# Optimization experiments

Measured on AMD Instinct MI355X. Metric: run time of the kernel, lower is better.

The kernel has to match this reference:

```python
import jax, jax.numpy as jnp
import numpy as np

B, S, DM, H = 16, 4096, 512, 4
HD = DM // H  # head_dim = 128
EPS = 1e-5


def setup_inputs() -> dict:
    key = jax.random.key(0)
    ks = jax.random.split(key, 9)
    sc = 1.0 / np.sqrt(DM)
    inp = {
        "x": jax.random.normal(ks[0], (B, S, DM), dtype=jnp.float32),
        "Wq_w": jax.random.normal(ks[1], (DM, DM), dtype=jnp.float32) * sc,
        "Wq_b": jnp.zeros((DM,), dtype=jnp.float32),
        "Wk_w": jax.random.normal(ks[2], (DM, DM), dtype=jnp.float32) * sc,
        "Wk_b": jnp.zeros((DM,), dtype=jnp.float32),
        "Wv_w": jax.random.normal(ks[3], (DM, DM), dtype=jnp.float32) * sc,
        "Wv_b": jnp.zeros((DM,), dtype=jnp.float32),
        "Wo_w": jax.random.normal(ks[4], (DM, DM), dtype=jnp.float32) * sc,
        "Wo_b": jnp.zeros((DM,), dtype=jnp.float32),
        "ln_g": jnp.ones((DM,), dtype=jnp.float32),
        "ln_b": jnp.zeros((DM,), dtype=jnp.float32),
    }
    return inp


def _forward(x, Wq_w, Wq_b, Wk_w, Wk_b, Wv_w, Wv_b, Wo_w, Wo_b, ln_g, ln_b):
    b, s, _ = x.shape
    # Linear projections, viewed as [B,S,H,HD] exactly as the torch code does
    Q = (x @ Wq_w.T + Wq_b).reshape(b, s, H, HD)
    K = (x @ Wk_w.T + Wk_b).reshape(b, s, H, HD)
    V = (x @ Wv_w.T + Wv_b).reshape(b, s, H, HD)
    # NOTE: source never permutes heads to dim 1, so attention is over the
    # HEAD axis per token: scores [B,S,H,H]
    scores = jnp.einsum("bshd,bstd->bsht", Q, K) / np.sqrt(HD).astype(np.float32)
    attn = jax.nn.softmax(scores, axis=-1)  # dropout is identity in eval
    out = jnp.einsum("bsht,bstd->bshd", attn, V).reshape(b, s, DM)
    out = out @ Wo_w.T + Wo_b
    y = out + x  # input_dim == output_dim -> residual branch taken
    mu = jnp.mean(y, axis=-1, keepdims=True)
    var = jnp.mean((y - mu) ** 2, axis=-1, keepdims=True)
    return (y - mu) * jax.lax.rsqrt(var + EPS) * ln_g + ln_b


def reference(x, Wq_w, Wq_b, Wk_w, Wk_b, Wv_w, Wv_b, Wo_w, Wo_b, ln_g, ln_b):
    return _forward(x, Wq_w, Wq_b, Wk_w, Wk_b, Wv_w, Wv_b, Wo_w, Wo_b, ln_g, ln_b)
```

## Files before the change

kernel.cpp:

```cpp
#include <hip/hip_runtime.h>
#include <stdint.h>

#define NTOK 65536
#define DMODEL 512
#define QKVN 1536
#define LN_EPS 1e-5f

typedef __attribute__((ext_vector_type(8))) short short8;
typedef __attribute__((ext_vector_type(8))) unsigned short ushort8;
typedef __attribute__((ext_vector_type(4))) float float4_t;
typedef __attribute__((ext_vector_type(4))) unsigned int uint4_t;

static __device__ __forceinline__ float bf2f(unsigned short u) {
    union { unsigned int i; float f; } c; c.i = ((unsigned int)u) << 16; return c.f;
}
static __device__ __forceinline__ unsigned short f2bf(float f) {
    union { float f; unsigned int i; } c; c.f = f;
    unsigned int x = c.i;
    return (unsigned short)((x + 0x7fffu + ((x >> 16) & 1u)) >> 16);
}
static __device__ __forceinline__ unsigned int cvt_pk_bf16(float lo, float hi) {
    unsigned int r;
    asm("v_cvt_pk_bf16_f32 %0, %1, %2" : "=v"(r) : "v"(lo), "v"(hi));
    return r;
}
static __device__ __forceinline__ void gload_lds16(const void* g, void* l) {
    __builtin_amdgcn_global_load_lds((const __attribute__((address_space(1))) void*)g,
                                     (__attribute__((address_space(3))) void*)l, 16, 0, 0);
}

#define BAR() __builtin_amdgcn_s_barrier()
#define WAITL0() asm volatile("s_waitcnt lgkmcnt(0)" ::: "memory")
#define WVM(n) asm volatile("s_waitcnt vmcnt(" #n ")" ::: "memory")
#define MFMA(a, b, c) __builtin_amdgcn_mfma_f32_16x16x32_bf16((a), (b), (c), 0, 0, 0)

__global__ __launch_bounds__(256) void cast_x_kernel(const float* __restrict__ x,
                                                     unsigned short* __restrict__ xb, int n8) {
    int stride = gridDim.x * blockDim.x;
    for (int i = blockIdx.x * blockDim.x + threadIdx.x; i < n8; i += stride) {
        const float4_t* p = (const float4_t*)(x + (size_t)i * 8);
        float4_t a = p[0], b = p[1];
        ushort8 v;
        v[0] = f2bf(a[0]); v[1] = f2bf(a[1]); v[2] = f2bf(a[2]); v[3] = f2bf(a[3]);
        v[4] = f2bf(b[0]); v[5] = f2bf(b[1]); v[6] = f2bf(b[2]); v[7] = f2bf(b[3]);
        *(ushort8*)(xb + (size_t)i * 8) = v;
    }
}

__global__ __launch_bounds__(256) void prep_w_kernel(
    const float* __restrict__ wq, const float* __restrict__ wk, const float* __restrict__ wv,
    const float* __restrict__ wo,
    const float* __restrict__ bq, const float* __restrict__ bk, const float* __restrict__ bv,
    unsigned short* __restrict__ wqkv, unsigned short* __restrict__ wpack,
    float* __restrict__ bias_qkv) {
    const int WN = DMODEL * DMODEL;
    int tid = blockIdx.x * blockDim.x + threadIdx.x;
    int stride = gridDim.x * blockDim.x;
    for (int j = tid; j < 3 * WN; j += stride) {
        int seg = j / WN, idx = j - seg * WN;
        const float* src = (seg == 0) ? wq : (seg == 1) ? wk : wv;
        wqkv[j] = f2bf(src[idx]);
    }
    for (int j = tid; j < WN; j += stride) {
        int e = j & 7, l = (j >> 3) & 63, nf = (j >> 9) & 31, kt = j >> 14;
        int row = nf * 16 + (l & 15);
        int k = kt * 32 + ((l >> 4) << 3) + e;
        wpack[j] = f2bf(wo[row * 512 + k]);
    }
    for (int j = tid; j < QKVN; j += stride)
        bias_qkv[j] = (j < 512) ? bq[j] : (j < 1024) ? bk[j - 512] : bv[j - 1024];
}

__global__ __launch_bounds__(512, 2) void gemm1_kernel(
    const unsigned short* __restrict__ A, const unsigned short* __restrict__ Bw,
    const float* __restrict__ bias, unsigned short* __restrict__ Cout) {
    __shared__ unsigned short As[4][256 * 32];
    __shared__ unsigned short Bs[4][256 * 32];

    const int b = blockIdx.x;
    const int L = (b & 7) * 192 + (b >> 3);
    const int bm = L / 6;
    const int bn = L - bm * 6;

    const int t = threadIdx.x;
    const int lane = t & 63;
    const int w = t >> 6;
    const int wm = w >> 2, wn = w & 3;

    const unsigned short* Ab = A + (size_t)bm * 256 * 512;
    const unsigned short* Bb = Bw + (size_t)bn * 256 * 512;

    const int i0 = t, i1 = 512 + t;
    const int r0 = i0 >> 2, s0 = (i0 & 3) ^ ((r0 >> 1) & 3);
    const int r1 = i1 >> 2, s1 = (i1 & 3) ^ ((r1 >> 1) & 3);

#define STAGE_A1(kt) do { \
        gload_lds16(Ab + r0 * 512 + (kt) * 32 + s0 * 8, &As[(kt) & 3][i0 * 8]); \
        gload_lds16(Ab + r1 * 512 + (kt) * 32 + s1 * 8, &As[(kt) & 3][i1 * 8]); } while (0)
#define STAGE_B1(kt) do { \
        gload_lds16(Bb + r0 * 512 + (kt) * 32 + s0 * 8, &Bs[(kt) & 3][i0 * 8]); \
        gload_lds16(Bb + r1 * 512 + (kt) * 32 + s1 * 8, &Bs[(kt) & 3][i1 * 8]); } while (0)

    int aoff[8], boff[4];
#pragma unroll
    for (int m = 0; m < 8; m++) {
        int row = wm * 128 + m * 16 + (lane & 15);
        aoff[m] = row * 32 + (((lane >> 4) ^ ((row >> 1) & 3)) * 8);
    }
#pragma unroll
    for (int n = 0; n < 4; n++) {
        int row = wn * 64 + n * 16 + (lane & 15);
        boff[n] = row * 32 + (((lane >> 4) ^ ((row >> 1) & 3)) * 8);
    }

    float4_t acc[8][4];
#pragma unroll
    for (int m = 0; m < 8; m++)
#pragma unroll
        for (int n = 0; n < 4; n++) acc[m][n] = (float4_t){0.f, 0.f, 0.f, 0.f};

    STAGE_A1(0); STAGE_B1(0);
    STAGE_A1(1); STAGE_B1(1);
    STAGE_A1(2); STAGE_B1(2);
    WVM(8);
    BAR();

    short8 ar[8], br[4];
#pragma unroll
    for (int kt = 0; kt < 16; ++kt) {
        const int sl = kt & 3;
#pragma unroll
        for (int m = 0; m < 8; m++) ar[m] = *(const short8*)&As[sl][aoff[m]];
        br[0] = *(const short8*)&Bs[sl][boff[0]];
        br[1] = *(const short8*)&Bs[sl][boff[1]];
        if (kt <= 12) STAGE_A1(kt + 3);
        BAR();
        WAITL0();
        __builtin_amdgcn_s_setprio(1);
#pragma unroll
        for (int m = 0; m < 8; m++) {
            acc[m][0] = MFMA(ar[m], br[0], acc[m][0]);
            acc[m][1] = MFMA(ar[m], br[1], acc[m][1]);
        }
        __builtin_amdgcn_s_setprio(0);
        BAR();
        br[2] = *(const short8*)&Bs[sl][boff[2]];
        br[3] = *(const short8*)&Bs[sl][boff[3]];
        if (kt <= 12) STAGE_B1(kt + 3);
        BAR();
        WAITL0();
        __builtin_amdgcn_s_setprio(1);
#pragma unroll
        for (int m = 0; m < 8; m++) {
            acc[m][2] = MFMA(ar[m], br[2], acc[m][2]);
            acc[m][3] = MFMA(ar[m], br[3], acc[m][3]);
        }
        __builtin_amdgcn_s_setprio(0);
        if (kt <= 12) { WVM(8); }
        else if (kt == 13) { WVM(4); }
        else if (kt == 14) { WVM(0); }
        BAR();
    }

    const int orow0 = bm * 256 + wm * 128;
    const int ocol0 = bn * 256 + wn * 64;
#pragma unroll
    for (int m = 0; m < 8; m++) {
#pragma unroll
        for (int n = 0; n < 4; n++) {
            int col = ocol0 + n * 16 + (lane & 15);
            float bv = bias[col];
#pragma unroll
            for (int j = 0; j < 4; j++) {
                int row = orow0 + m * 16 + (lane >> 4) * 4 + j;
                Cout[(size_t)row * QKVN + col] = f2bf(acc[m][n][j] + bv);
            }
        }
    }
#undef STAGE_A1
#undef STAGE_B1
}

__global__ __launch_bounds__(256, 4) void attn_o_ln_kernel(
    const unsigned short* __restrict__ qkv, const unsigned short* __restrict__ Wpack,
    const float* __restrict__ bo, const float* __restrict__ xres,
    const float* __restrict__ lng, const float* __restrict__ lnb,
    float* __restrict__ Y) {
    __shared__ __align__(16) unsigned char AOs[32 * 1024];
    float* red = (float*)AOs;

    const int T0 = blockIdx.x * 32;
    const int t = threadIdx.x;
    const int lane = t & 63;
    const int w = t >> 6;
    const int g = lane >> 4;
    const int sl = lane & 15;

    const float scale = 0.08838834764831845f;

#pragma unroll 1
    for (int r = 0; r < 2; ++r) {
        const int tr = w * 8 + r * 4 + g;
        const unsigned short* base = qkv + (size_t)(T0 + tr) * QKVN + sl * 8;

        short8 qr[4], kr[4], vr[4];
#pragma unroll
        for (int h = 0; h < 4; h++) {
            qr[h] = *(const short8*)(base + h * 128);
            kr[h] = *(const short8*)(base + 512 + h * 128);
            vr[h] = *(const short8*)(base + 1024 + h * 128);
        }
#pragma unroll
        for (int h = 0; h < 4; h++) {
            float qf[8];
#pragma unroll
            for (int d = 0; d < 8; d++) qf[d] = bf2f((unsigned short)qr[h][d]);
            float s[4];
#pragma unroll
            for (int tt = 0; tt < 4; tt++) {
                float a0 = 0.f;
#pragma unroll
                for (int d = 0; d < 8; d++) a0 += qf[d] * bf2f((unsigned short)kr[tt][d]);
                s[tt] = a0;
            }
#pragma unroll
            for (int mask = 1; mask < 16; mask <<= 1)
#pragma unroll
                for (int tt = 0; tt < 4; tt++)
                    s[tt] += __shfl_xor(s[tt], mask, 64);
            float m0 = fmaxf(fmaxf(s[0], s[1]), fmaxf(s[2], s[3])) * scale;
            float p[4];
            float sum = 0.f;
#pragma unroll
            for (int tt = 0; tt < 4; tt++) { p[tt] = __expf(s[tt] * scale - m0); sum += p[tt]; }
            float rr = __frcp_rn(sum);
            float o[8];
#pragma unroll
            for (int d = 0; d < 8; d++) o[d] = 0.f;
#pragma unroll
            for (int tt = 0; tt < 4; tt++) {
                float ph = p[tt] * rr;
#pragma unroll
                for (int d = 0; d < 8; d++) o[d] += ph * bf2f((unsigned short)vr[tt][d]);
            }
            uint4_t pk;
            pk[0] = cvt_pk_bf16(o[0], o[1]);
            pk[1] = cvt_pk_bf16(o[2], o[3]);
            pk[2] = cvt_pk_bf16(o[4], o[5]);
            pk[3] = cvt_pk_bf16(o[6], o[7]);
            int off = tr * 1024 + ((h * 256 + sl * 16) ^ ((tr & 7) << 4));
            *(uint4_t*)(AOs + off) = pk;
        }
    }
    __syncthreads();

    const unsigned short* Bb2 = Wpack + ((size_t)(w * 8) * 64 + lane) * 8;
    const int arow0 = sl;
    const int arow1 = 16 + sl;

    float4_t acc[2][8];
#pragma unroll
    for (int m = 0; m < 2; m++)
#pragma unroll
        for (int n = 0; n < 8; n++) acc[m][n] = (float4_t){0.f, 0.f, 0.f, 0.f};

#pragma unroll 1
    for (int kt = 0; kt < 16; ++kt) {
        short8 bfr[8];
#pragma unroll
        for (int n = 0; n < 8; n++)
            bfr[n] = *(const short8*)(Bb2 + (size_t)kt * 16384 + n * 512);
        int lslot = kt * 64 + g * 16;
        short8 a0 = *(const short8*)(AOs + arow0 * 1024 + (lslot ^ ((arow0 & 7) << 4)));
        short8 a1 = *(const short8*)(AOs + arow1 * 1024 + (lslot ^ ((arow1 & 7) << 4)));
#pragma unroll
        for (int n = 0; n < 8; n++) {
            acc[0][n] = MFMA(a0, bfr[n], acc[0][n]);
            acc[1][n] = MFMA(a1, bfr[n], acc[1][n]);
        }
    }
    __syncthreads();

    float bias8[8], gc8[8], bc8[8];
#pragma unroll
    for (int n = 0; n < 8; n++) {
        int c = w * 128 + n * 16 + sl;
        bias8[n] = bo[c]; gc8[n] = lng[c]; bc8[n] = lnb[c];
    }
#pragma unroll
    for (int m = 0; m < 2; m++) {
#pragma unroll
        for (int j = 0; j < 4; j++) {
            int grow = T0 + m * 16 + g * 4 + j;
            const float* xr = xres + (size_t)grow * 512;
#pragma unroll
            for (int n = 0; n < 8; n++)
                acc[m][n][j] += bias8[n] + xr[w * 128 + n * 16 + sl];
        }
    }
#pragma unroll
    for (int m = 0; m < 2; m++) {
#pragma unroll
        for (int j = 0; j < 4; j++) {
            float s = 0.f, s2 = 0.f;
#pragma unroll
            for (int n = 0; n < 8; n++) { float v = acc[m][n][j]; s += v; s2 += v * v; }
#pragma unroll
            for (int mask = 1; mask < 16; mask <<= 1) {
                s += __shfl_xor(s, mask, 64);
                s2 += __shfl_xor(s2, mask, 64);
            }
            if (sl == 0) {
                int rl = m * 16 + g * 4 + j;
                red[(rl * 4 + w) * 2 + 0] = s;
                red[(rl * 4 + w) * 2 + 1] = s2;
            }
        }
    }
    __syncthreads();
#pragma unroll
    for (int m = 0; m < 2; m++) {
#pragma unroll
        for (int j = 0; j < 4; j++) {
            int rl = m * 16 + g * 4 + j;
            float s = 0.f, s2 = 0.f;
#pragma unroll
            for (int i = 0; i < 4; i++) {
                s += red[(rl * 4 + i) * 2 + 0];
                s2 += red[(rl * 4 + i) * 2 + 1];
            }
            float mu = s * (1.f / 512.f);
            float var = s2 * (1.f / 512.f) - mu * mu;
            float inv = rsqrtf(var + LN_EPS);
            float* yp = Y + (size_t)(T0 + rl) * 512;
#pragma unroll
            for (int n = 0; n < 8; n++) {
                int c = w * 128 + n * 16 + sl;
                yp[c] = (acc[m][n][j] - mu) * inv * gc8[n] + bc8[n];
            }
        }
    }
}

extern "C" void kernel_launch(void* const* d_in, const int* in_sizes, int n_in,
                              void* d_out, int out_size, void* d_ws, size_t ws_size,
                              hipStream_t stream) {
    const float* x   = (const float*)d_in[0];
    const float* wq  = (const float*)d_in[1];
    const float* bq  = (const float*)d_in[2];
    const float* wk  = (const float*)d_in[3];
    const float* bk  = (const float*)d_in[4];
    const float* wv  = (const float*)d_in[5];
    const float* bv  = (const float*)d_in[6];
    const float* wo  = (const float*)d_in[7];
    const float* bo  = (const float*)d_in[8];
    const float* lng = (const float*)d_in[9];
    const float* lnb = (const float*)d_in[10];

    char* ws = (char*)d_ws;
    unsigned short* Xb    = (unsigned short*)(ws);
    unsigned short* Wqkv  = (unsigned short*)(ws + 67108864);
    unsigned short* Wpack = (unsigned short*)(ws + 68681728);
    float*          Bqkv  = (float*)        (ws + 69206016);
    unsigned short* QKV   = (unsigned short*)(ws + 69212160);
    float* Y = (float*)d_out;

    cast_x_kernel<<<2048, 256, 0, stream>>>(x, Xb, NTOK * 512 / 8);
    prep_w_kernel<<<1024, 256, 0, stream>>>(wq, wk, wv, wo, bq, bk, bv, Wqkv, Wpack, Bqkv);

    gemm1_kernel<<<(NTOK / 256) * (QKVN / 256), 512, 0, stream>>>(Xb, Wqkv, Bqkv, QKV);

    attn_o_ln_kernel<<<NTOK / 32, 256, 0, stream>>>(QKV, Wpack, bo, x, lng, lnb, Y);
}
```

Baseline: 381.3 us.

## Use 512 threads in attn_o_ln kernel, splitting warps over rows and columns

Doubles the block size of the fused attention/out-projection/LayerNorm kernel to 8 waves. Each wave now handles 4 tokens in the head-attention phase and one 16-row by 128-column tile in the MFMA phase, instead of 8 tokens and 32 rows. This halves per-thread accumulators and sequential attention work, lowering register pressure and raising parallelism. The cost is that each wave reloads the Wo fragments for its column slice, doubling B-operand global reads per block. The attention loop also reloads K and V inside the per-head loop, adding redundant loads.

```diff
diff --git a/kernel.cpp b/kernel.cpp
--- a/kernel.cpp
+++ b/kernel.cpp
@@ -181,7 +181,7 @@
 #undef STAGE_B1
 }
 
-__global__ __launch_bounds__(256, 4) void attn_o_ln_kernel(
+__global__ __launch_bounds__(512, 4) void attn_o_ln_kernel(
     const unsigned short* __restrict__ qkv, const unsigned short* __restrict__ Wpack,
     const float* __restrict__ bo, const float* __restrict__ xres,
     const float* __restrict__ lng, const float* __restrict__ lnb,
@@ -195,26 +195,31 @@
     const int w = t >> 6;
     const int g = lane >> 4;
     const int sl = lane & 15;
+    const int wm = w >> 2;
+    const int wn = w & 3;
 
     const float scale = 0.08838834764831845f;
 
-#pragma unroll 1
-    for (int r = 0; r < 2; ++r) {
-        const int tr = w * 8 + r * 4 + g;
+    {
+        const int tr = w * 4 + g;
         const unsigned short* base = qkv + (size_t)(T0 + tr) * QKVN + sl * 8;
 
-        short8 qr[4], kr[4], vr[4];
 #pragma unroll
         for (int h = 0; h < 4; h++) {
-            qr[h] = *(const short8*)(base + h * 128);
-            kr[h] = *(const short8*)(base + 512 + h * 128);
-            vr[h] = *(const short8*)(base + 1024 + h * 128);
-        }
-#pragma unroll
-        for (int h = 0; h < 4; h++) {
+            short8 qr = *(const short8*)(base + h * 128);
+            short8 kr[4];
+            kr[0] = *(const short8*)(base + 512 + h * 128);
+            short8 vr[4];
+            vr[0] = *(const short8*)(base + 1024 + h * 128);
+            kr[1] = kr[0]; vr[1] = vr[0];
+#pragma unroll
+            for (int tt = 0; tt < 4; tt++) {
+                kr[tt] = *(const short8*)(base + 512 + tt * 128);
+                vr[tt] = *(const short8*)(base + 1024 + tt * 128);
+            }
             float qf[8];
 #pragma unroll
-            for (int d = 0; d < 8; d++) qf[d] = bf2f((unsigned short)qr[h][d]);
+            for (int d = 0; d < 8; d++) qf[d] = bf2f((unsigned short)qr[d]);
             float s[4];
 #pragma unroll
             for (int tt = 0; tt < 4; tt++) {
@@ -254,15 +259,12 @@
     }
     __syncthreads();
 
-    const unsigned short* Bb2 = Wpack + ((size_t)(w * 8) * 64 + lane) * 8;
-    const int arow0 = sl;
-    const int arow1 = 16 + sl;
-
-    float4_t acc[2][8];
-#pragma unroll
-    for (int m = 0; m < 2; m++)
-#pragma unroll
-        for (int n = 0; n < 8; n++) acc[m][n] = (float4_t){0.f, 0.f, 0.f, 0.f};
+    const unsigned short* Bb2 = Wpack + ((size_t)(wn * 8) * 64 + lane) * 8;
+    const int arow = wm * 16 + sl;
+
+    float4_t acc[8];
+#pragma unroll
+    for (int n = 0; n < 8; n++) acc[n] = (float4_t){0.f, 0.f, 0.f, 0.f};
 
 #pragma unroll 1
     for (int kt = 0; kt < 16; ++kt) {
@@ -271,73 +273,60 @@
         for (int n = 0; n < 8; n++)
             bfr[n] = *(const short8*)(Bb2 + (size_t)kt * 16384 + n * 512);
         int lslot = kt * 64 + g * 16;
-        short8 a0 = *(const short8*)(AOs + arow0 * 1024 + (lslot ^ ((arow0 & 7) << 4)));
-        short8 a1 = *(const short8*)(AOs + arow1 * 1024 + (lslot ^ ((arow1 & 7) << 4)));
+        short8 a0 = *(const short8*)(AOs + arow * 1024 + (lslot ^ ((arow & 7) << 4)));
+#pragma unroll
+        for (int n = 0; n < 8; n++) acc[n] = MFMA(a0, bfr[n], acc[n]);
+    }
+    __syncthreads();
+
+    float bias8[8], gc8[8], bc8[8];
+#pragma unroll
+    for (int n = 0; n < 8; n++) {
+        int c = wn * 128 + n * 16 + sl;
+        bias8[n] = bo[c]; gc8[n] = lng[c]; bc8[n] = lnb[c];
+    }
+#pragma unroll
+    for (int j = 0; j < 4; j++) {
+        int grow = T0 + wm * 16 + g * 4 + j;
+        const float* xr = xres + (size_t)grow * 512;
+#pragma unroll
+        for (int n = 0; n < 8; n++)
+            acc[n][j] += bias8[n] + xr[wn * 128 + n * 16 + sl];
+    }
+#pragma unroll
+    for (int j = 0; j < 4; j++) {
+        float s = 0.f, s2 = 0.f;
+#pragma unroll
+        for (int n = 0; n < 8; n++) { float v = acc[n][j]; s += v; s2 += v * v; }
+#pragma unroll
+        for (int mask = 1; mask < 16; mask <<= 1) {
+            s += __shfl_xor(s, mask, 64);
+            s2 += __shfl_xor(s2, mask, 64);
+        }
+        if (sl == 0) {
+            int rl = wm * 16 + g * 4 + j;
+            red[(rl * 4 + wn) * 2 + 0] = s;
+            red[(rl * 4 + wn) * 2 + 1] = s2;
+        }
+    }
+    __syncthreads();
+#pragma unroll
+    for (int j = 0; j < 4; j++) {
+        int rl = wm * 16 + g * 4 + j;
+        float s = 0.f, s2 = 0.f;
+#pragma unroll
+        for (int i = 0; i < 4; i++) {
+            s += red[(rl * 4 + i) * 2 + 0];
+            s2 += red[(rl * 4 + i) * 2 + 1];
+        }
+        float mu = s * (1.f / 512.f);
+        float var = s2 * (1.f / 512.f) - mu * mu;
+        float inv = rsqrtf(var + LN_EPS);
+        float* yp = Y + (size_t)(T0 + rl) * 512;
 #pragma unroll
         for (int n = 0; n < 8; n++) {
-            acc[0][n] = MFMA(a0, bfr[n], acc[0][n]);
-            acc[1][n] = MFMA(a1, bfr[n], acc[1][n]);
-        }
-    }
-    __syncthreads();
-
-    float bias8[8], gc8[8], bc8[8];
-#pragma unroll
-    for (int n = 0; n < 8; n++) {
-        int c = w * 128 + n * 16 + sl;
-        bias8[n] = bo[c]; gc8[n] = lng[c]; bc8[n] = lnb[c];
-    }
-#pragma unroll
-    for (int m = 0; m < 2; m++) {
-#pragma unroll
-        for (int j = 0; j < 4; j++) {
-            int grow = T0 + m * 16 + g * 4 + j;
-            const float* xr = xres + (size_t)grow * 512;
-#pragma unroll
-            for (int n = 0; n < 8; n++)
-                acc[m][n][j] += bias8[n] + xr[w * 128 + n * 16 + sl];
-        }
-    }
-#pragma unroll
-    for (int m = 0; m < 2; m++) {
-#pragma unroll
-        for (int j = 0; j < 4; j++) {
-            float s = 0.f, s2 = 0.f;
-#pragma unroll
-            for (int n = 0; n < 8; n++) { float v = acc[m][n][j]; s += v; s2 += v * v; }
-#pragma unroll
-            for (int mask = 1; mask < 16; mask <<= 1) {
-                s += __shfl_xor(s, mask, 64);
-                s2 += __shfl_xor(s2, mask, 64);
-            }
-            if (sl == 0) {
-                int rl = m * 16 + g * 4 + j;
-                red[(rl * 4 + w) * 2 + 0] = s;
-                red[(rl * 4 + w) * 2 + 1] = s2;
-            }
-        }
-    }
-    __syncthreads();
-#pragma unroll
-    for (int m = 0; m < 2; m++) {
-#pragma unroll
-        for (int j = 0; j < 4; j++) {
-            int rl = m * 16 + g * 4 + j;
-            float s = 0.f, s2 = 0.f;
-#pragma unroll
-            for (int i = 0; i < 4; i++) {
-                s += red[(rl * 4 + i) * 2 + 0];
-                s2 += red[(rl * 4 + i) * 2 + 1];
-            }
-            float mu = s * (1.f / 512.f);
-            float var = s2 * (1.f / 512.f) - mu * mu;
-            float inv = rsqrtf(var + LN_EPS);
-            float* yp = Y + (size_t)(T0 + rl) * 512;
-#pragma unroll
-            for (int n = 0; n < 8; n++) {
-                int c = w * 128 + n * 16 + sl;
-                yp[c] = (acc[m][n][j] - mu) * inv * gc8[n] + bc8[n];
-            }
+            int c = wn * 128 + n * 16 + sl;
+            yp[c] = (acc[n][j] - mu) * inv * gc8[n] + bc8[n];
         }
     }
 }
@@ -370,5 +359,5 @@
 
     gemm1_kernel<<<(NTOK / 256) * (QKVN / 256), 512, 0, stream>>>(Xb, Wqkv, Bqkv, QKV);
 
-    attn_o_ln_kernel<<<NTOK / 32, 256, 0, stream>>>(QKV, Wpack, bo, x, lng, lnb, Y);
-}
+    attn_o_ln_kernel<<<NTOK / 32, 512, 0, stream>>>(QKV, Wpack, bo, x, lng, lnb, Y);
+}
```

Result: faster. 333.0 us (-12.7%).

## Stage Wo tiles in double-buffered LDS and widen attention block to 64 tokens

Applied to the files above, without the earlier changes.

The fused attention/output-projection/LayerNorm kernel now handles 64 tokens per block with 8 waves (2x4 wave grid) instead of 32 tokens with 4 waves. Wo is no longer pre-packed for direct per-wave global fragment loads. Instead it is cast to plain bf16 and streamed into swizzled, double-buffered shared memory with async global-to-LDS loads, overlapping the next k-tile load with MFMA work. The aim is to share each Wo tile across two row-groups of waves, halving redundant global/L2 traffic for weights. In exchange it adds per-k-tile barriers and more LDS per block, which can lower occupancy.

```diff
diff --git a/kernel.cpp b/kernel.cpp
--- a/kernel.cpp
+++ b/kernel.cpp
@@ -51,7 +51,7 @@
     const float* __restrict__ wq, const float* __restrict__ wk, const float* __restrict__ wv,
     const float* __restrict__ wo,
     const float* __restrict__ bq, const float* __restrict__ bk, const float* __restrict__ bv,
-    unsigned short* __restrict__ wqkv, unsigned short* __restrict__ wpack,
+    unsigned short* __restrict__ wqkv, unsigned short* __restrict__ wob,
     float* __restrict__ bias_qkv) {
     const int WN = DMODEL * DMODEL;
     int tid = blockIdx.x * blockDim.x + threadIdx.x;
@@ -61,12 +61,7 @@
         const float* src = (seg == 0) ? wq : (seg == 1) ? wk : wv;
         wqkv[j] = f2bf(src[idx]);
     }
-    for (int j = tid; j < WN; j += stride) {
-        int e = j & 7, l = (j >> 3) & 63, nf = (j >> 9) & 31, kt = j >> 14;
-        int row = nf * 16 + (l & 15);
-        int k = kt * 32 + ((l >> 4) << 3) + e;
-        wpack[j] = f2bf(wo[row * 512 + k]);
-    }
+    for (int j = tid; j < WN; j += stride) wob[j] = f2bf(wo[j]);
     for (int j = tid; j < QKVN; j += stride)
         bias_qkv[j] = (j < 512) ? bq[j] : (j < 1024) ? bk[j - 512] : bv[j - 1024];
 }
@@ -181,24 +176,37 @@
 #undef STAGE_B1
 }
 
-__global__ __launch_bounds__(256, 4) void attn_o_ln_kernel(
-    const unsigned short* __restrict__ qkv, const unsigned short* __restrict__ Wpack,
+__global__ __launch_bounds__(512, 2) void attn_gemm_ln_kernel(
+    const unsigned short* __restrict__ qkv, const unsigned short* __restrict__ Wob,
     const float* __restrict__ bo, const float* __restrict__ xres,
     const float* __restrict__ lng, const float* __restrict__ lnb,
     float* __restrict__ Y) {
-    __shared__ __align__(16) unsigned char AOs[32 * 1024];
-    float* red = (float*)AOs;
-
-    const int T0 = blockIdx.x * 32;
+    __shared__ __align__(16) unsigned char AOs[64 * 1024];
+    __shared__ __align__(16) unsigned char Bsm[2][32768];
+    float* red = (float*)Bsm;
+
+    const int T0 = blockIdx.x * 64;
     const int t = threadIdx.x;
     const int lane = t & 63;
     const int w = t >> 6;
     const int g = lane >> 4;
     const int sl = lane & 15;
+    const int wm = w >> 2;
+    const int wn = w & 3;
+
+#define STAGE_B2(kt) do { \
+        _Pragma("unroll") \
+        for (int c = 0; c < 4; c++) { \
+            int idx = c * 512 + t; \
+            int row = idx >> 2; \
+            int s = (idx & 3) ^ ((row >> 1) & 3); \
+            gload_lds16(Wob + row * 512 + (kt) * 32 + s * 8, &Bsm[(kt) & 1][idx * 16]); \
+        } } while (0)
+
+    STAGE_B2(0);
 
     const float scale = 0.08838834764831845f;
-
-#pragma unroll 1
+#pragma unroll
     for (int r = 0; r < 2; ++r) {
         const int tr = w * 8 + r * 4 + g;
         const unsigned short* base = qkv + (size_t)(T0 + tr) * QKVN + sl * 8;
@@ -254,9 +262,16 @@
     }
     __syncthreads();
 
-    const unsigned short* Bb2 = Wpack + ((size_t)(w * 8) * 64 + lane) * 8;
-    const int arow0 = sl;
-    const int arow1 = 16 + sl;
+    const int arow0 = wm * 32 + sl;
+    const int arow1 = wm * 32 + 16 + sl;
+    const int aswz0 = (arow0 & 7) << 4;
+    const int aswz1 = (arow1 & 7) << 4;
+    int boffB[8];
+#pragma unroll
+    for (int n = 0; n < 8; n++) {
+        int row = wn * 128 + n * 16 + sl;
+        boffB[n] = row * 64 + ((g ^ ((row >> 1) & 3)) * 16);
+    }
 
     float4_t acc[2][8];
 #pragma unroll
@@ -266,36 +281,39 @@
 
 #pragma unroll 1
     for (int kt = 0; kt < 16; ++kt) {
-        short8 bfr[8];
-#pragma unroll
-        for (int n = 0; n < 8; n++)
-            bfr[n] = *(const short8*)(Bb2 + (size_t)kt * 16384 + n * 512);
-        int lslot = kt * 64 + g * 16;
-        short8 a0 = *(const short8*)(AOs + arow0 * 1024 + (lslot ^ ((arow0 & 7) << 4)));
-        short8 a1 = *(const short8*)(AOs + arow1 * 1024 + (lslot ^ ((arow1 & 7) << 4)));
+        if (kt < 15) { STAGE_B2(kt + 1); WVM(4); }
+        else { WVM(0); }
+        BAR();
+        const unsigned char* Bp = Bsm[kt & 1];
+        short8 a0 = *(const short8*)(AOs + arow0 * 1024 + ((kt * 64 + g * 16) ^ aswz0));
+        short8 a1 = *(const short8*)(AOs + arow1 * 1024 + ((kt * 64 + g * 16) ^ aswz1));
+        __builtin_amdgcn_s_setprio(1);
 #pragma unroll
         for (int n = 0; n < 8; n++) {
-            acc[0][n] = MFMA(a0, bfr[n], acc[0][n]);
-            acc[1][n] = MFMA(a1, bfr[n], acc[1][n]);
-        }
+            short8 bf = *(const short8*)(Bp + boffB[n]);
+            acc[0][n] = MFMA(a0, bf, acc[0][n]);
+            acc[1][n] = MFMA(a1, bf, acc[1][n]);
+        }
+        __builtin_amdgcn_s_setprio(0);
+        BAR();
     }
     __syncthreads();
 
     float bias8[8], gc8[8], bc8[8];
 #pragma unroll
     for (int n = 0; n < 8; n++) {
-        int c = w * 128 + n * 16 + sl;
+        int c = wn * 128 + n * 16 + sl;
         bias8[n] = bo[c]; gc8[n] = lng[c]; bc8[n] = lnb[c];
     }
 #pragma unroll
     for (int m = 0; m < 2; m++) {
 #pragma unroll
         for (int j = 0; j < 4; j++) {
-            int grow = T0 + m * 16 + g * 4 + j;
+            int grow = T0 + wm * 32 + m * 16 + g * 4 + j;
             const float* xr = xres + (size_t)grow * 512;
 #pragma unroll
             for (int n = 0; n < 8; n++)
-                acc[m][n][j] += bias8[n] + xr[w * 128 + n * 16 + sl];
+                acc[m][n][j] += bias8[n] + xr[wn * 128 + n * 16 + sl];
         }
     }
 #pragma unroll
@@ -311,9 +329,9 @@
                 s2 += __shfl_xor(s2, mask, 64);
             }
             if (sl == 0) {
-                int rl = m * 16 + g * 4 + j;
-                red[(rl * 4 + w) * 2 + 0] = s;
-                red[(rl * 4 + w) * 2 + 1] = s2;
+                int rl = wm * 32 + m * 16 + g * 4 + j;
+                red[(rl * 4 + wn) * 2 + 0] = s;
+                red[(rl * 4 + wn) * 2 + 1] = s2;
             }
         }
     }
@@ -322,7 +340,7 @@
     for (int m = 0; m < 2; m++) {
 #pragma unroll
         for (int j = 0; j < 4; j++) {
-            int rl = m * 16 + g * 4 + j;
+            int rl = wm * 32 + m * 16 + g * 4 + j;
             float s = 0.f, s2 = 0.f;
 #pragma unroll
             for (int i = 0; i < 4; i++) {
@@ -335,11 +353,12 @@
             float* yp = Y + (size_t)(T0 + rl) * 512;
 #pragma unroll
             for (int n = 0; n < 8; n++) {
-                int c = w * 128 + n * 16 + sl;
+                int c = wn * 128 + n * 16 + sl;
                 yp[c] = (acc[m][n][j] - mu) * inv * gc8[n] + bc8[n];
             }
         }
     }
+#undef STAGE_B2
 }
 
 extern "C" void kernel_launch(void* const* d_in, const int* in_sizes, int n_in,
@@ -360,15 +379,15 @@
     char* ws = (char*)d_ws;
     unsigned short* Xb    = (unsigned short*)(ws);
     unsigned short* Wqkv  = (unsigned short*)(ws + 67108864);
-    unsigned short* Wpack = (unsigned short*)(ws + 68681728);
+    unsigned short* Wob   = (unsigned short*)(ws + 68681728);
     float*          Bqkv  = (float*)        (ws + 69206016);
     unsigned short* QKV   = (unsigned short*)(ws + 69212160);
     float* Y = (float*)d_out;
 
     cast_x_kernel<<<2048, 256, 0, stream>>>(x, Xb, NTOK * 512 / 8);
-    prep_w_kernel<<<1024, 256, 0, stream>>>(wq, wk, wv, wo, bq, bk, bv, Wqkv, Wpack, Bqkv);
+    prep_w_kernel<<<1024, 256, 0, stream>>>(wq, wk, wv, wo, bq, bk, bv, Wqkv, Wob, Bqkv);
 
     gemm1_kernel<<<(NTOK / 256) * (QKVN / 256), 512, 0, stream>>>(Xb, Wqkv, Bqkv, QKV);
 
-    attn_o_ln_kernel<<<NTOK / 32, 256, 0, stream>>>(QKV, Wpack, bo, x, lng, lnb, Y);
-}
+    attn_gemm_ln_kernel<<<NTOK / 64, 512, 0, stream>>>(QKV, Wob, bo, x, lng, lnb, Y);
+}
```

After: 322.7 us. 1.18x faster.
